# Kernel optimization log

Measured on AMD Instinct MI355X. Metric: run time of the kernel, lower is better.

## Reference

```python
import jax, jax.numpy as jnp
import numpy as np

EPS = 1e-5  # torch BatchNorm2d default eps


def _conv(x, w, b, pad):
    y = jax.lax.conv_general_dilated(
        x, w, window_strides=(1, 1), padding=[(pad, pad), (pad, pad)],
        dimension_numbers=('NCHW', 'OIHW', 'NCHW'))
    return y + b[None, :, None, None]


def _bn_train(x, gamma, beta):
    # training-mode BatchNorm2d: biased batch statistics over (N,H,W)
    m = jnp.mean(x, axis=(0, 2, 3), keepdims=True)
    v = jnp.var(x, axis=(0, 2, 3), keepdims=True)
    xn = (x - m) * jax.lax.rsqrt(v + EPS)
    return xn * gamma[None, :, None, None] + beta[None, :, None, None]


def _ncc(s, t):
    # Vectorized equivalent of the per-pixel double loop.
    # ncc[b,0,i,j] = mean(tt * ss / (tt_std * ss_std)) over (C,th,tw)
    #             = sum(tt * s_sub) / (N * tt_std * ss_std)   (since sum(tt)=0)
    b, c, sh, sw = s.shape
    th, tw = t.shape[2], t.shape[3]
    N = c * th * tw
    tt = t - jnp.mean(t, axis=(1, 2, 3), keepdims=True)
    # torch.std is unbiased (divides by N-1)
    tt_std = jnp.sqrt(jnp.sum(tt * tt, axis=(1, 2, 3), keepdims=True) / (N - 1))

    # cross[b] = valid correlation of s[b] with its own template tt[b]
    def per_sample(si, ti):
        return jax.lax.conv_general_dilated(
            si[None], ti[None], (1, 1), 'VALID',
            dimension_numbers=('NCHW', 'OIHW', 'NCHW'))[0]  # (1,h,w)

    cross = jax.vmap(per_sample)(s, tt)  # (b,1,h,w)

    # per-window mean/std of s via box-filter conv over all C channels jointly
    box = jnp.ones((1, c, th, tw), dtype=s.dtype)
    win_sum = jax.lax.conv_general_dilated(
        s, box, (1, 1), 'VALID', dimension_numbers=('NCHW', 'OIHW', 'NCHW'))
    win_sqsum = jax.lax.conv_general_dilated(
        s * s, box, (1, 1), 'VALID', dimension_numbers=('NCHW', 'OIHW', 'NCHW'))
    win_mean = win_sum / N
    ss_var = jnp.maximum(win_sqsum - N * win_mean * win_mean, 0.0) / (N - 1)
    ss_std = jnp.sqrt(ss_var)

    return cross / (N * tt_std * ss_std)  # (b,1,h,w)


def reference(s, t, w1, b1, g1, be1, w2, b2, g2, be2,
              w3, b3, g3, be3, w4, b4):
    s = _bn_train(_conv(s, w1, b1, pad=1), g1, be1)
    t = _bn_train(_conv(t, w2, b2, pad=1), g2, be2)
    ncc = _ncc(s, t)
    x = _bn_train(_conv(ncc, w3, b3, pad=0), g3, be3)
    x = jax.nn.relu(x)
    return _conv(x, w4, b4, pad=0)  # (b,2,h,w)


def setup_inputs() -> dict:
    key = jax.random.key(0)
    ks = jax.random.split(key, 12)
    C = 256
    inp = {
        's': jax.random.normal(ks[0], (16, C, 64, 64), jnp.float32),
        't': jax.random.normal(ks[1], (16, C, 16, 16), jnp.float32),
        'w1': jax.random.normal(ks[2], (C, C, 3, 3), jnp.float32) * 0.02,
        'b1': jax.random.normal(ks[3], (C,), jnp.float32) * 0.02,
        'g1': jnp.ones((C,), jnp.float32),
        'be1': jnp.zeros((C,), jnp.float32),
        'w2': jax.random.normal(ks[4], (C, C, 3, 3), jnp.float32) * 0.02,
        'b2': jax.random.normal(ks[5], (C,), jnp.float32) * 0.02,
        'g2': jnp.ones((C,), jnp.float32),
        'be2': jnp.zeros((C,), jnp.float32),
        'w3': jax.random.normal(ks[6], (1, 1, 1, 1), jnp.float32),
        'b3': jax.random.normal(ks[7], (1,), jnp.float32) * 0.02,
        'g3': jnp.ones((1,), jnp.float32),
        'be3': jnp.zeros((1,), jnp.float32),
        'w4': jax.random.normal(ks[8], (2, 1, 1, 1), jnp.float32),
        'b4': jax.random.normal(ks[9], (2,), jnp.float32) * 0.02,
    }
    return inp
```

## Files before the change

### kernel.cpp

```cpp
#include <hip/hip_runtime.h>
#include <hip/hip_bf16.h>

#define EPSV 1e-5f

constexpr int B_ = 16, C_ = 256;
constexpr int OHW_ = 49 * 49;
constexpr int NTOT = 256 * 16 * 16;
constexpr int GROUPS = 32, CPERG = 8;

typedef short bf16x8 __attribute__((ext_vector_type(8)));
typedef float f32x4 __attribute__((ext_vector_type(4)));

constexpr size_t OFF_S1 = 0;
constexpr size_t SZ_S1  = (size_t)16 * 256 * 4096;
constexpr size_t OFF_T2 = OFF_S1 + SZ_S1;
constexpr size_t SZ_T2  = (size_t)16 * 256 * 256;
constexpr size_t OFF_ST = OFF_T2 + SZ_T2;
constexpr size_t OFF_C  = OFF_ST + 2048;
constexpr size_t SPC_BYTES = (size_t)16 * 66 * 66 * 256 * 2;
constexpr size_t TPC_BYTES = (size_t)16 * 18 * 18 * 256 * 2;
constexpr size_t WR_BYTES  = (size_t)9 * 256 * 256 * 2;
constexpr size_t ZOFF  = 0;
constexpr size_t CPOFF = 131072;
constexpr size_t NCOFF = CPOFF + (size_t)GROUPS * 16 * OHW_;
constexpr size_t SATOFF = NCOFF + (size_t)16 * OHW_;

__device__ __forceinline__ void gload_lds16(const void* g, void* l) {
    __builtin_amdgcn_global_load_lds((const __attribute__((address_space(1))) unsigned int*)g,
                                     (__attribute__((address_space(3))) unsigned int*)l,
                                     16, 0, 0);
}

template<int W>
__global__ __launch_bounds__(256)
void pad_transpose(const float* __restrict__ in, __hip_bfloat16* __restrict__ outp)
{
    constexpr int PW = W + 2;
    __shared__ float tile[64][W + 1];
    int bid = blockIdx.x;
    int icg = bid & 3; bid >>= 2;
    int yp = bid % PW; bid /= PW;
    int b = bid;
    int ic0 = icg * 64;
    int tid = threadIdx.x;
    bool interior = (yp >= 1 && yp <= W);
    if (interior) {
        int y = yp - 1;
        for (int idx = tid; idx < 64 * W; idx += 256) {
            int i = idx / W, x = idx % W;
            tile[i][x] = in[(((size_t)(b * C_ + ic0 + i)) * W + y) * W + x];
        }
    }
    __syncthreads();
    for (int idx = tid; idx < PW * 16; idx += 256) {
        int xp = idx >> 4, i4 = idx & 15;
        ushort4 v = make_ushort4(0, 0, 0, 0);
        if (interior && xp >= 1 && xp <= W) {
            #pragma unroll
            for (int k = 0; k < 4; ++k) {
                __hip_bfloat16 h = __float2bfloat16(tile[i4 * 4 + k][xp - 1]);
                reinterpret_cast<unsigned short*>(&v)[k] = *reinterpret_cast<unsigned short*>(&h);
            }
        }
        *reinterpret_cast<ushort4*>(&outp[(((size_t)(b * PW) + yp) * PW + xp) * 256 + ic0 + i4 * 4]) = v;
    }
}

__global__ __launch_bounds__(256)
void weight_reorg(const float* __restrict__ w, __hip_bfloat16* __restrict__ wr)
{
    int idx = blockIdx.x * 256 + threadIdx.x;
    const float* src = w + (size_t)idx * 9;
    #pragma unroll
    for (int t = 0; t < 9; ++t)
        wr[(size_t)t * 65536 + idx] = __float2bfloat16(src[t]);
}

template<int W>
__global__ __launch_bounds__(256, 3)
void conv_mfma(const __hip_bfloat16* __restrict__ SPc, const __hip_bfloat16* __restrict__ Wr,
               const float* __restrict__ bias, float* __restrict__ out,
               float* __restrict__ csum, float* __restrict__ csq)
{
    constexpr int PW = W + 2;
    constexpr int NPIX = W * W;
    constexpr int NT = NPIX / 128;
    constexpr int NWG = 16 * 2 * NT;
    constexpr int CHUNK = NWG / 8;
    constexpr int NK = 72;
    __shared__ __hip_bfloat16 A_lds[3][128 * 32];
    __shared__ __hip_bfloat16 B_lds[3][128 * 32];

    int logical = (blockIdx.x & 7) * CHUNK + (blockIdx.x >> 3);
    int nt = logical % NT; logical /= NT;
    int mt = logical & 1;  logical >>= 1;
    int b  = logical;
    int tid = threadIdx.x;
    int lane = tid & 63;
    int wv = tid >> 6, wm = wv >> 1, wn = wv & 1;
    int oc0 = mt * 128, p0 = nt * 128;

    f32x4 acc[4][4];
    #pragma unroll
    for (int i = 0; i < 4; ++i)
        #pragma unroll
        for (int j = 0; j < 4; ++j)
            #pragma unroll
            for (int r = 0; r < 4; ++r) acc[i][j][r] = 0.f;

    int colb = lane >> 4;
    int rA = lane & 15;

    const __hip_bfloat16* baseA[2];
    const __hip_bfloat16* baseB[2];
    #pragma unroll
    for (int it = 0; it < 2; ++it) {
        int sIdx = tid + it * 256;
        int row = sIdx >> 2, seg = sIdx & 3;
        baseA[it] = Wr + ((size_t)(oc0 + row)) * 256 + seg * 8;
        int p = p0 + row;
        int y = p / W, x = p % W;
        baseB[it] = SPc + (((size_t)(b * PW + y)) * PW + x) * 256 + seg * 8;
    }

    auto STAGE = [&](int buf, int kc) {
        int tap = kc >> 3, icc = kc & 7;
        int offA = tap * 65536 + icc * 32;
        int offB = ((tap / 3) * PW + (tap % 3)) * 256 + icc * 32;
        #pragma unroll
        for (int it = 0; it < 2; ++it) {
            int sIdx = tid + it * 256;
            gload_lds16(baseA[it] + offA, &A_lds[buf][sIdx * 8]);
            gload_lds16(baseB[it] + offB, &B_lds[buf][sIdx * 8]);
        }
    };

    STAGE(0, 0);
    STAGE(1, 1);

    for (int k = 0; k < NK; ++k) {
        int cur = k % 3;
        if (k + 2 < NK) { asm volatile("s_waitcnt vmcnt(4)" ::: "memory"); }
        else            { asm volatile("s_waitcnt vmcnt(0)" ::: "memory"); }
        __builtin_amdgcn_s_barrier();
        asm volatile("" ::: "memory");

        const bf16x8* Af = reinterpret_cast<const bf16x8*>(&A_lds[cur][0]);
        const bf16x8* Bf = reinterpret_cast<const bf16x8*>(&B_lds[cur][0]);
        bf16x8 a[4], bb[4];
        #pragma unroll
        for (int mi = 0; mi < 4; ++mi)
            a[mi] = Af[(wm * 64 + mi * 16 + rA) * 4 + colb];
        #pragma unroll
        for (int ni = 0; ni < 4; ++ni)
            bb[ni] = Bf[(wn * 64 + ni * 16 + rA) * 4 + colb];
        #pragma unroll
        for (int mi = 0; mi < 4; ++mi)
            #pragma unroll
            for (int ni = 0; ni < 4; ++ni)
                acc[mi][ni] = __builtin_amdgcn_mfma_f32_16x16x32_bf16(
                    a[mi], bb[ni], acc[mi][ni], 0, 0, 0);

        if (k + 2 < NK) STAGE((k + 2) % 3, k + 2);
    }

    #pragma unroll
    for (int mi = 0; mi < 4; ++mi) {
        int ocb = oc0 + wm * 64 + mi * 16 + (lane >> 4) * 4;
        #pragma unroll
        for (int r = 0; r < 4; ++r) {
            int oc = ocb + r;
            float bv = bias[oc];
            float* orow = out + ((size_t)(b * C_ + oc)) * NPIX;
            float s_oc = 0.f, q_oc = 0.f;
            #pragma unroll
            for (int ni = 0; ni < 4; ++ni) {
                int px = p0 + wn * 64 + ni * 16 + (lane & 15);
                float v = acc[mi][ni][r] + bv;
                orow[px] = v;
                s_oc += v; q_oc += v * v;
            }
            #pragma unroll
            for (int m_ = 1; m_ < 16; m_ <<= 1) {
                s_oc += __shfl_xor(s_oc, m_);
                q_oc += __shfl_xor(q_oc, m_);
            }
            if ((lane & 15) == 0) {
                atomicAdd(&csum[oc], s_oc);
                atomicAdd(&csq[oc], q_oc);
            }
        }
    }
}

__device__ inline void blk_reduce2(float& a, float& q, int tid) {
    #pragma unroll
    for (int off = 32; off > 0; off >>= 1) {
        a += __shfl_down(a, off);
        q += __shfl_down(q, off);
    }
    __shared__ float ra[4], rq[4];
    if ((tid & 63) == 0) { ra[tid >> 6] = a; rq[tid >> 6] = q; }
    __syncthreads();
    if (tid == 0) { a = ra[0] + ra[1] + ra[2] + ra[3]; q = rq[0] + rq[1] + rq[2] + rq[3]; }
}

__global__ __launch_bounds__(256)
void bn_norm(float* __restrict__ x, const float* __restrict__ csum,
             const float* __restrict__ csq, const float* __restrict__ g,
             const float* __restrict__ be, int HW, int total4, float inv_cnt)
{
    int i = blockIdx.x * 256 + threadIdx.x;
    if (i >= total4) return;
    int c = ((i * 4) / HW) % C_;
    float m = csum[c] * inv_cnt;
    float v = csq[c] * inv_cnt - m * m;
    float sc = rsqrtf(v + EPSV) * g[c];
    float sh = be[c] - m * sc;
    float4 val = reinterpret_cast<float4*>(x)[i];
    val.x = val.x * sc + sh;
    val.y = val.y * sc + sh;
    val.z = val.z * sc + sh;
    val.w = val.w * sc + sh;
    reinterpret_cast<float4*>(x)[i] = val;
}

__global__ __launch_bounds__(256)
void zplane_kernel(const float* __restrict__ s1, const float* __restrict__ csum,
                   const float* __restrict__ csq, const float* __restrict__ g1,
                   const float* __restrict__ be1, float* __restrict__ z)
{
    __shared__ float SC[256], SH[256];
    int tid = threadIdx.x;
    {
        float m = csum[tid] * (1.f / 65536.f);
        float v = csq[tid] * (1.f / 65536.f) - m * m;
        float sc = rsqrtf(v + EPSV) * g1[tid];
        SC[tid] = sc; SH[tid] = be1[tid] - m * sc;
    }
    __syncthreads();
    int i4 = blockIdx.x * 256 + tid;
    int b = i4 >> 10, p4 = i4 & 1023;
    const float4* base = reinterpret_cast<const float4*>(s1 + (size_t)b * (C_ * 4096)) + p4;
    float4 s = make_float4(0.f, 0.f, 0.f, 0.f);
    float4 q = make_float4(0.f, 0.f, 0.f, 0.f);
    for (int c = 0; c < C_; ++c) {
        float4 v = base[(size_t)c * 1024];
        float sc = SC[c], sh = SH[c];
        float vx = v.x * sc + sh, vy = v.y * sc + sh, vz = v.z * sc + sh, vw = v.w * sc + sh;
        s.x += vx; s.y += vy; s.z += vz; s.w += vw;
        q.x += vx * vx; q.y += vy * vy; q.z += vz * vz; q.w += vw * vw;
    }
    reinterpret_cast<float4*>(z)[i4] = s;
    reinterpret_cast<float4*>(z + 65536)[i4] = q;
}

__global__ __launch_bounds__(256)
void sat_kernel(const float* __restrict__ zin, float* __restrict__ sat)
{
    __shared__ float t[65][66];
    int pl = blockIdx.x;
    int tid = threadIdx.x;
    const float* src = zin + (size_t)pl * 4096;
    for (int idx = tid; idx < 4096; idx += 256) {
        int y = idx >> 6, x = idx & 63;
        t[y + 1][x + 1] = src[idx];
    }
    for (int idx = tid; idx < 65; idx += 256) { t[0][idx] = 0.f; t[idx][0] = 0.f; }
    __syncthreads();
    if (tid < 64) {
        float run = 0.f;
        for (int x = 1; x <= 64; ++x) { run += t[tid + 1][x]; t[tid + 1][x] = run; }
    }
    __syncthreads();
    if (tid < 64) {
        float run = 0.f;
        for (int y = 1; y <= 64; ++y) { run += t[y][tid + 1]; t[y][tid + 1] = run; }
    }
    __syncthreads();
    float* dst = sat + (size_t)pl * 4225;
    for (int idx = tid; idx < 4225; idx += 256) {
        int r = idx / 65, c = idx % 65;
        dst[idx] = t[r][c];
    }
}

__global__ __launch_bounds__(256)
void tstat_kernel(const float* __restrict__ t2, float* __restrict__ tmean, float* __restrict__ ttstd)
{
    int b = blockIdx.x, tid = threadIdx.x;
    const float* p = t2 + (size_t)b * NTOT;
    float s = 0.f, q = 0.f;
    for (int i = tid; i < NTOT; i += 256) { float v = p[i]; s += v; q += v * v; }
    blk_reduce2(s, q, tid);
    if (tid == 0) {
        float m = s / (float)NTOT;
        tmean[b] = m;
        ttstd[b] = sqrtf(fmaxf(q - (float)NTOT * m * m, 0.f) / (float)(NTOT - 1));
    }
}

__global__ __launch_bounds__(256, 2)
void cross_v3(const float* __restrict__ s1, const float* __restrict__ t2,
              const float* __restrict__ csum, const float* __restrict__ csq,
              const float* __restrict__ g1, const float* __restrict__ be1,
              float* __restrict__ cpart)
{
    __shared__ float4 spl4[1024];
    __shared__ float tpl[256];
    __shared__ float red[4][64][49];

    int g = blockIdx.x & (GROUPS - 1);
    int b = blockIdx.x / GROUPS;
    int tid = threadIdx.x;
    int phase = tid >> 6;
    int lane = tid & 63;
    int i = lane;
    int i_ld = i < 49 ? i : 48;

    float acc[49];
    #pragma unroll
    for (int j = 0; j < 49; ++j) acc[j] = 0.f;

    #pragma unroll 1
    for (int cc = 0; cc < CPERG; ++cc) {
        int c = g * CPERG + cc;
        float m = csum[c] * (1.f / 65536.f);
        float v = csq[c] * (1.f / 65536.f) - m * m;
        float sc = rsqrtf(v + EPSV) * g1[c];
        float sh = be1[c] - m * sc;
        __syncthreads();
        const float4* sp4 = reinterpret_cast<const float4*>(s1 + ((size_t)(b * C_ + c)) * 4096);
        #pragma unroll
        for (int k = 0; k < 4; ++k) {
            int gidx = tid + k * 256;
            float4 val = sp4[gidx];
            val.x = val.x * sc + sh; val.y = val.y * sc + sh;
            val.z = val.z * sc + sh; val.w = val.w * sc + sh;
            int row = gidx >> 4, jg = gidx & 15;
            spl4[row * 16 + (jg ^ (row & 7))] = val;
        }
        tpl[tid] = t2[((size_t)(b * C_ + c)) * 256 + tid];
        __syncthreads();
        #pragma unroll 1
        for (int tyl = 0; tyl < 4; ++tyl) {
            int ty = phase * 4 + tyl;
            int row = i_ld + ty;
            float r_[64];
            #pragma unroll
            for (int jg = 0; jg < 16; ++jg) {
                float4 v4 = spl4[row * 16 + (jg ^ (row & 7))];
                r_[jg * 4 + 0] = v4.x; r_[jg * 4 + 1] = v4.y;
                r_[jg * 4 + 2] = v4.z; r_[jg * 4 + 3] = v4.w;
            }
            float tt[16];
            const float4* tp4 = reinterpret_cast<const float4*>(&tpl[ty * 16]);
            #pragma unroll
            for (int k = 0; k < 4; ++k) {
                float4 tv = tp4[k];
                tt[k * 4 + 0] = tv.x; tt[k * 4 + 1] = tv.y;
                tt[k * 4 + 2] = tv.z; tt[k * 4 + 3] = tv.w;
            }
            #pragma unroll
            for (int tx = 0; tx < 16; ++tx)
                #pragma unroll
                for (int j = 0; j < 49; ++j)
                    acc[j] += tt[tx] * r_[j + tx];
        }
    }
    __syncthreads();
    if (i < 49) {
        #pragma unroll
        for (int j = 0; j < 49; ++j) red[phase][i][j] = acc[j];
    }
    __syncthreads();
    float* dst = cpart + ((size_t)(g * B_ + b)) * OHW_;
    for (int e = tid; e < OHW_; e += 256) {
        int ii = e / 49, jj = e - ii * 49;
        dst[e] = red[0][ii][jj] + red[1][ii][jj] + red[2][ii][jj] + red[3][ii][jj];
    }
}

__global__ __launch_bounds__(256)
void ncc_kernel(const float* __restrict__ cpart, const float* __restrict__ sat,
                const float* __restrict__ tmean, const float* __restrict__ ttstd,
                float* __restrict__ ncc, float* __restrict__ s3)
{
    int idx = blockIdx.x * 256 + threadIdx.x;
    float val = 0.f;
    if (idx < B_ * OHW_) {
        int b = idx / OHW_, r = idx - b * OHW_;
        int i = r / 49, j = r - i * 49;
        float cr = 0.f;
        #pragma unroll 4
        for (int g = 0; g < GROUPS; ++g) cr += cpart[((size_t)(g * B_ + b)) * OHW_ + r];
        const float* sz = sat + (size_t)b * 4225;
        const float* sq = sat + (size_t)(16 + b) * 4225;
        int a00 = i * 65 + j, a01 = i * 65 + j + 16;
        int a10 = (i + 16) * 65 + j, a11 = (i + 16) * 65 + j + 16;
        float wsum = sz[a11] - sz[a01] - sz[a10] + sz[a00];
        float wq   = sq[a11] - sq[a01] - sq[a10] + sq[a00];
        float crosst = cr - tmean[b] * wsum;
        float ssvar = fmaxf(wq - wsum * wsum * (1.f / 65536.f), 0.f) * (1.f / 65535.f);
        float ssstd = sqrtf(ssvar);
        val = crosst / (65536.f * ttstd[b] * ssstd);
        ncc[idx] = val;
    }
    float s = val, q = val * val;
    blk_reduce2(s, q, threadIdx.x);
    if (threadIdx.x == 0) { atomicAdd(&s3[0], s); atomicAdd(&s3[1], q); }
}

__global__ __launch_bounds__(256)
void final_kernel(const float* __restrict__ ncc, const float* __restrict__ s3,
                  const float* __restrict__ w3, const float* __restrict__ b3,
                  const float* __restrict__ g3, const float* __restrict__ be3,
                  const float* __restrict__ w4, const float* __restrict__ b4,
                  float* __restrict__ out)
{
    int idx = blockIdx.x * 256 + threadIdx.x;
    if (idx >= B_ * OHW_) return;
    constexpr float M = (float)(B_ * OHW_);
    float mn = s3[0] / M;
    float vn = s3[1] / M - mn * mn;
    float W3 = w3[0], B3 = b3[0];
    float my = W3 * mn + B3;
    float vy = W3 * W3 * vn;
    float sc = rsqrtf(vy + EPSV) * g3[0];
    float y = (W3 * ncc[idx] + B3 - my) * sc + be3[0];
    float h = fmaxf(y, 0.f);
    int b = idx / OHW_, r = idx - b * OHW_;
    out[((size_t)(b * 2 + 0)) * OHW_ + r] = h * w4[0] + b4[0];
    out[((size_t)(b * 2 + 1)) * OHW_ + r] = h * w4[1] + b4[1];
}

extern "C" void kernel_launch(void* const* d_in, const int* in_sizes, int n_in,
                              void* d_out, int out_size, void* d_ws, size_t ws_size,
                              hipStream_t stream)
{
    const float* s   = (const float*)d_in[0];
    const float* t   = (const float*)d_in[1];
    const float* w1  = (const float*)d_in[2];
    const float* b1  = (const float*)d_in[3];
    const float* g1  = (const float*)d_in[4];
    const float* be1 = (const float*)d_in[5];
    const float* w2  = (const float*)d_in[6];
    const float* b2  = (const float*)d_in[7];
    const float* g2  = (const float*)d_in[8];
    const float* be2 = (const float*)d_in[9];
    const float* w3  = (const float*)d_in[10];
    const float* b3  = (const float*)d_in[11];
    const float* g3  = (const float*)d_in[12];
    const float* be3 = (const float*)d_in[13];
    const float* w4  = (const float*)d_in[14];
    const float* b4  = (const float*)d_in[15];

    float* ws = (float*)d_ws;
    float* S1 = ws + OFF_S1;
    float* T2 = ws + OFF_T2;
    float* ST = ws + OFF_ST;
    float* CHS1 = ST + 0;
    float* CHQ1 = ST + 256;
    float* CHS2 = ST + 512;
    float* CHQ2 = ST + 768;
    float* S3   = ST + 1024;
    float* TM   = ST + 1040;
    float* TSD  = ST + 1056;

    char* Cb = (char*)(ws + OFF_C);
    __hip_bfloat16* SPc = (__hip_bfloat16*)Cb;
    __hip_bfloat16* TPc = (__hip_bfloat16*)(Cb + SPC_BYTES);
    __hip_bfloat16* Wr1 = (__hip_bfloat16*)(Cb + SPC_BYTES + TPC_BYTES);
    __hip_bfloat16* Wr2 = (__hip_bfloat16*)(Cb + SPC_BYTES + TPC_BYTES + WR_BYTES);
    float* Cf = (float*)Cb;
    float* Z   = Cf + ZOFF;
    float* CP  = Cf + CPOFF;
    float* NC  = Cf + NCOFF;
    float* SAT = Cf + SATOFF;

    hipMemsetAsync(ST, 0, 1026 * sizeof(float), stream);

    pad_transpose<64><<<dim3(16 * 66 * 4), dim3(256), 0, stream>>>(s, SPc);
    pad_transpose<16><<<dim3(16 * 18 * 4), dim3(256), 0, stream>>>(t, TPc);
    weight_reorg<<<dim3(256), dim3(256), 0, stream>>>(w1, Wr1);
    weight_reorg<<<dim3(256), dim3(256), 0, stream>>>(w2, Wr2);

    conv_mfma<64><<<dim3(16 * 2 * 32), dim3(256), 0, stream>>>(SPc, Wr1, b1, S1, CHS1, CHQ1);
    conv_mfma<16><<<dim3(16 * 2 * 2),  dim3(256), 0, stream>>>(TPc, Wr2, b2, T2, CHS2, CHQ2);

    bn_norm<<<dim3(1024), dim3(256), 0, stream>>>(T2, CHS2, CHQ2, g2, be2, 256, 262144, 1.f / 4096.f);
    tstat_kernel<<<dim3(16), dim3(256), 0, stream>>>(T2, TM, TSD);

    zplane_kernel<<<dim3(64), dim3(256), 0, stream>>>(S1, CHS1, CHQ1, g1, be1, Z);
    sat_kernel<<<dim3(32), dim3(256), 0, stream>>>(Z, SAT);

    cross_v3<<<dim3(16 * GROUPS), dim3(256), 0, stream>>>(S1, T2, CHS1, CHQ1, g1, be1, CP);
    ncc_kernel<<<dim3(151), dim3(256), 0, stream>>>(CP, SAT, TM, TSD, NC, S3);
    final_kernel<<<dim3(151), dim3(256), 0, stream>>>(NC, S3, w3, b3, g3, be3, w4, b4, (float*)d_out);
}
```

Measured before the change: 513.3 us.

## Merge launches, fuse z-plane sums into cross kernel, double-buffer conv

After: 453.4 us. 11.7% less time.

```diff
diff --git a/kernel.cpp b/kernel.cpp
--- a/kernel.cpp
+++ b/kernel.cpp
@@ -16,12 +16,12 @@
 constexpr size_t OFF_T2 = OFF_S1 + SZ_S1;
 constexpr size_t SZ_T2  = (size_t)16 * 256 * 256;
 constexpr size_t OFF_ST = OFF_T2 + SZ_T2;
-constexpr size_t OFF_C  = OFF_ST + 2048;
+constexpr size_t OFF_Z  = OFF_ST + 2048;
+constexpr size_t OFF_C  = OFF_Z + 131072;
 constexpr size_t SPC_BYTES = (size_t)16 * 66 * 66 * 256 * 2;
 constexpr size_t TPC_BYTES = (size_t)16 * 18 * 18 * 256 * 2;
 constexpr size_t WR_BYTES  = (size_t)9 * 256 * 256 * 2;
-constexpr size_t ZOFF  = 0;
-constexpr size_t CPOFF = 131072;
+constexpr size_t CPOFF = 0;
 constexpr size_t NCOFF = CPOFF + (size_t)GROUPS * 16 * OHW_;
 constexpr size_t SATOFF = NCOFF + (size_t)16 * OHW_;
 
@@ -32,12 +32,10 @@
 }
 
 template<int W>
-__global__ __launch_bounds__(256)
-void pad_transpose(const float* __restrict__ in, __hip_bfloat16* __restrict__ outp)
+__device__ __forceinline__ void pad_body(int bid, const float* __restrict__ in,
+                                         __hip_bfloat16* __restrict__ outp, float* tile)
 {
     constexpr int PW = W + 2;
-    __shared__ float tile[64][W + 1];
-    int bid = blockIdx.x;
     int icg = bid & 3; bid >>= 2;
     int yp = bid % PW; bid /= PW;
     int b = bid;
@@ -48,7 +46,7 @@
         int y = yp - 1;
         for (int idx = tid; idx < 64 * W; idx += 256) {
             int i = idx / W, x = idx % W;
-            tile[i][x] = in[(((size_t)(b * C_ + ic0 + i)) * W + y) * W + x];
+            tile[i * (W + 1) + x] = in[(((size_t)(b * C_ + ic0 + i)) * W + y) * W + x];
         }
     }
     __syncthreads();
@@ -58,7 +56,7 @@
         if (interior && xp >= 1 && xp <= W) {
             #pragma unroll
             for (int k = 0; k < 4; ++k) {
-                __hip_bfloat16 h = __float2bfloat16(tile[i4 * 4 + k][xp - 1]);
+                __hip_bfloat16 h = __float2bfloat16(tile[(i4 * 4 + k) * (W + 1) + xp - 1]);
                 reinterpret_cast<unsigned short*>(&v)[k] = *reinterpret_cast<unsigned short*>(&h);
             }
         }
@@ -67,9 +65,22 @@
 }
 
 __global__ __launch_bounds__(256)
-void weight_reorg(const float* __restrict__ w, __hip_bfloat16* __restrict__ wr)
-{
-    int idx = blockIdx.x * 256 + threadIdx.x;
+void pad_all(const float* __restrict__ s, const float* __restrict__ t,
+             __hip_bfloat16* __restrict__ SPc, __hip_bfloat16* __restrict__ TPc)
+{
+    __shared__ float tile[64 * 65];
+    if (blockIdx.x < 16 * 66 * 4) pad_body<64>(blockIdx.x, s, SPc, tile);
+    else                          pad_body<16>(blockIdx.x - 16 * 66 * 4, t, TPc, tile);
+}
+
+__global__ __launch_bounds__(256)
+void weight_reorg_all(const float* __restrict__ w1, const float* __restrict__ w2,
+                      __hip_bfloat16* __restrict__ wr1, __hip_bfloat16* __restrict__ wr2)
+{
+    int bb = blockIdx.x;
+    const float* w = (bb < 256) ? w1 : w2;
+    __hip_bfloat16* wr = (bb < 256) ? wr1 : wr2;
+    int idx = (bb & 255) * 256 + threadIdx.x;
     const float* src = w + (size_t)idx * 9;
     #pragma unroll
     for (int t = 0; t < 9; ++t)
@@ -77,21 +88,16 @@
 }
 
 template<int W>
-__global__ __launch_bounds__(256, 3)
-void conv_mfma(const __hip_bfloat16* __restrict__ SPc, const __hip_bfloat16* __restrict__ Wr,
-               const float* __restrict__ bias, float* __restrict__ out,
-               float* __restrict__ csum, float* __restrict__ csq)
+__device__ __forceinline__ void conv_body(
+    int logical,
+    const __hip_bfloat16* __restrict__ SPc, const __hip_bfloat16* __restrict__ Wr,
+    const float* __restrict__ bias, float* __restrict__ out,
+    float* __restrict__ csum, float* __restrict__ csq,
+    __hip_bfloat16 (&A_lds)[2][4096], __hip_bfloat16 (&B_lds)[2][4096])
 {
     constexpr int PW = W + 2;
     constexpr int NPIX = W * W;
     constexpr int NT = NPIX / 128;
-    constexpr int NWG = 16 * 2 * NT;
-    constexpr int CHUNK = NWG / 8;
-    constexpr int NK = 72;
-    __shared__ __hip_bfloat16 A_lds[3][128 * 32];
-    __shared__ __hip_bfloat16 B_lds[3][128 * 32];
-
-    int logical = (blockIdx.x & 7) * CHUNK + (blockIdx.x >> 3);
     int nt = logical % NT; logical /= NT;
     int mt = logical & 1;  logical >>= 1;
     int b  = logical;
@@ -108,9 +114,7 @@
             #pragma unroll
             for (int r = 0; r < 4; ++r) acc[i][j][r] = 0.f;
 
-    int colb = lane >> 4;
-    int rA = lane & 15;
-
+    int colb = lane >> 4, rA = lane & 15;
     const __hip_bfloat16* baseA[2];
     const __hip_bfloat16* baseB[2];
     #pragma unroll
@@ -136,14 +140,12 @@
     };
 
     STAGE(0, 0);
-    STAGE(1, 1);
-
-    for (int k = 0; k < NK; ++k) {
-        int cur = k % 3;
-        if (k + 2 < NK) { asm volatile("s_waitcnt vmcnt(4)" ::: "memory"); }
-        else            { asm volatile("s_waitcnt vmcnt(0)" ::: "memory"); }
-        __builtin_amdgcn_s_barrier();
-        asm volatile("" ::: "memory");
+    asm volatile("s_waitcnt vmcnt(0)" ::: "memory");
+    __syncthreads();
+
+    for (int kc = 0; kc < 72; ++kc) {
+        int cur = kc & 1;
+        if (kc + 1 < 72) STAGE(cur ^ 1, kc + 1);
 
         const bf16x8* Af = reinterpret_cast<const bf16x8*>(&A_lds[cur][0]);
         const bf16x8* Bf = reinterpret_cast<const bf16x8*>(&B_lds[cur][0]);
@@ -161,12 +163,12 @@
                 acc[mi][ni] = __builtin_amdgcn_mfma_f32_16x16x32_bf16(
                     a[mi], bb[ni], acc[mi][ni], 0, 0, 0);
 
-        if (k + 2 < NK) STAGE((k + 2) % 3, k + 2);
+        __syncthreads();
     }
 
     #pragma unroll
     for (int mi = 0; mi < 4; ++mi) {
-        int ocb = oc0 + wm * 64 + mi * 16 + (lane >> 4) * 4;
+        int ocb = oc0 + wm * 64 + mi * 16 + colb * 4;
         #pragma unroll
         for (int r = 0; r < 4; ++r) {
             int oc = ocb + r;
@@ -175,7 +177,7 @@
             float s_oc = 0.f, q_oc = 0.f;
             #pragma unroll
             for (int ni = 0; ni < 4; ++ni) {
-                int px = p0 + wn * 64 + ni * 16 + (lane & 15);
+                int px = p0 + wn * 64 + ni * 16 + rA;
                 float v = acc[mi][ni][r] + bv;
                 orow[px] = v;
                 s_oc += v; q_oc += v * v;
@@ -185,7 +187,7 @@
                 s_oc += __shfl_xor(s_oc, m_);
                 q_oc += __shfl_xor(q_oc, m_);
             }
-            if ((lane & 15) == 0) {
+            if (rA == 0) {
                 atomicAdd(&csum[oc], s_oc);
                 atomicAdd(&csq[oc], q_oc);
             }
@@ -193,6 +195,26 @@
     }
 }
 
+__global__ __launch_bounds__(256, 4)
+void conv_all(const __hip_bfloat16* __restrict__ SPc, const __hip_bfloat16* __restrict__ Wr1,
+              const float* __restrict__ b1, float* __restrict__ S1,
+              float* __restrict__ CHS1, float* __restrict__ CHQ1,
+              const __hip_bfloat16* __restrict__ TPc, const __hip_bfloat16* __restrict__ Wr2,
+              const float* __restrict__ b2, float* __restrict__ T2,
+              float* __restrict__ CHS2, float* __restrict__ CHQ2)
+{
+    __shared__ __hip_bfloat16 A_lds[2][4096];
+    __shared__ __hip_bfloat16 B_lds[2][4096];
+    int bid = blockIdx.x;
+    if (bid < 64) {
+        conv_body<16>(bid, TPc, Wr2, b2, T2, CHS2, CHQ2, A_lds, B_lds);
+    } else {
+        int l = bid - 64;
+        int logical = (l & 7) * 128 + (l >> 3);
+        conv_body<64>(logical, SPc, Wr1, b1, S1, CHS1, CHQ1, A_lds, B_lds);
+    }
+}
+
 __device__ inline void blk_reduce2(float& a, float& q, int tid) {
     #pragma unroll
     for (int off = 32; off > 0; off >>= 1) {
@@ -206,92 +228,32 @@
 }
 
 __global__ __launch_bounds__(256)
-void bn_norm(float* __restrict__ x, const float* __restrict__ csum,
-             const float* __restrict__ csq, const float* __restrict__ g,
-             const float* __restrict__ be, int HW, int total4, float inv_cnt)
-{
-    int i = blockIdx.x * 256 + threadIdx.x;
-    if (i >= total4) return;
-    int c = ((i * 4) / HW) % C_;
-    float m = csum[c] * inv_cnt;
-    float v = csq[c] * inv_cnt - m * m;
-    float sc = rsqrtf(v + EPSV) * g[c];
-    float sh = be[c] - m * sc;
-    float4 val = reinterpret_cast<float4*>(x)[i];
-    val.x = val.x * sc + sh;
-    val.y = val.y * sc + sh;
-    val.z = val.z * sc + sh;
-    val.w = val.w * sc + sh;
-    reinterpret_cast<float4*>(x)[i] = val;
-}
-
-__global__ __launch_bounds__(256)
-void zplane_kernel(const float* __restrict__ s1, const float* __restrict__ csum,
-                   const float* __restrict__ csq, const float* __restrict__ g1,
-                   const float* __restrict__ be1, float* __restrict__ z)
+void bn_t2_stats(float* __restrict__ T2, const float* __restrict__ csum,
+                 const float* __restrict__ csq, const float* __restrict__ g2,
+                 const float* __restrict__ be2, float* __restrict__ tmean,
+                 float* __restrict__ ttstd)
 {
     __shared__ float SC[256], SH[256];
-    int tid = threadIdx.x;
+    int b = blockIdx.x, tid = threadIdx.x;
     {
-        float m = csum[tid] * (1.f / 65536.f);
-        float v = csq[tid] * (1.f / 65536.f) - m * m;
-        float sc = rsqrtf(v + EPSV) * g1[tid];
-        SC[tid] = sc; SH[tid] = be1[tid] - m * sc;
-    }
-    __syncthreads();
-    int i4 = blockIdx.x * 256 + tid;
-    int b = i4 >> 10, p4 = i4 & 1023;
-    const float4* base = reinterpret_cast<const float4*>(s1 + (size_t)b * (C_ * 4096)) + p4;
-    float4 s = make_float4(0.f, 0.f, 0.f, 0.f);
-    float4 q = make_float4(0.f, 0.f, 0.f, 0.f);
-    for (int c = 0; c < C_; ++c) {
-        float4 v = base[(size_t)c * 1024];
+        float m = csum[tid] * (1.f / 4096.f);
+        float v = csq[tid] * (1.f / 4096.f) - m * m;
+        float sc = rsqrtf(v + EPSV) * g2[tid];
+        SC[tid] = sc; SH[tid] = be2[tid] - m * sc;
+    }
+    __syncthreads();
+    float4* p = reinterpret_cast<float4*>(T2 + (size_t)b * NTOT);
+    float s = 0.f, q = 0.f;
+    for (int i4 = tid; i4 < NTOT / 4; i4 += 256) {
+        int c = i4 >> 6;
         float sc = SC[c], sh = SH[c];
-        float vx = v.x * sc + sh, vy = v.y * sc + sh, vz = v.z * sc + sh, vw = v.w * sc + sh;
-        s.x += vx; s.y += vy; s.z += vz; s.w += vw;
-        q.x += vx * vx; q.y += vy * vy; q.z += vz * vz; q.w += vw * vw;
-    }
-    reinterpret_cast<float4*>(z)[i4] = s;
-    reinterpret_cast<float4*>(z + 65536)[i4] = q;
-}
-
-__global__ __launch_bounds__(256)
-void sat_kernel(const float* __restrict__ zin, float* __restrict__ sat)
-{
-    __shared__ float t[65][66];
-    int pl = blockIdx.x;
-    int tid = threadIdx.x;
-    const float* src = zin + (size_t)pl * 4096;
-    for (int idx = tid; idx < 4096; idx += 256) {
-        int y = idx >> 6, x = idx & 63;
-        t[y + 1][x + 1] = src[idx];
-    }
-    for (int idx = tid; idx < 65; idx += 256) { t[0][idx] = 0.f; t[idx][0] = 0.f; }
-    __syncthreads();
-    if (tid < 64) {
-        float run = 0.f;
-        for (int x = 1; x <= 64; ++x) { run += t[tid + 1][x]; t[tid + 1][x] = run; }
-    }
-    __syncthreads();
-    if (tid < 64) {
-        float run = 0.f;
-        for (int y = 1; y <= 64; ++y) { run += t[y][tid + 1]; t[y][tid + 1] = run; }
-    }
-    __syncthreads();
-    float* dst = sat + (size_t)pl * 4225;
-    for (int idx = tid; idx < 4225; idx += 256) {
-        int r = idx / 65, c = idx % 65;
-        dst[idx] = t[r][c];
-    }
-}
-
-__global__ __launch_bounds__(256)
-void tstat_kernel(const float* __restrict__ t2, float* __restrict__ tmean, float* __restrict__ ttstd)
-{
-    int b = blockIdx.x, tid = threadIdx.x;
-    const float* p = t2 + (size_t)b * NTOT;
-    float s = 0.f, q = 0.f;
-    for (int i = tid; i < NTOT; i += 256) { float v = p[i]; s += v; q += v * v; }
+        float4 v = p[i4];
+        v.x = v.x * sc + sh; v.y = v.y * sc + sh;
+        v.z = v.z * sc + sh; v.w = v.w * sc + sh;
+        s += v.x + v.y + v.z + v.w;
+        q += v.x * v.x + v.y * v.y + v.z * v.z + v.w * v.w;
+        p[i4] = v;
+    }
     blk_reduce2(s, q, tid);
     if (tid == 0) {
         float m = s / (float)NTOT;
@@ -304,7 +266,7 @@
 void cross_v3(const float* __restrict__ s1, const float* __restrict__ t2,
               const float* __restrict__ csum, const float* __restrict__ csq,
               const float* __restrict__ g1, const float* __restrict__ be1,
-              float* __restrict__ cpart)
+              float* __restrict__ cpart, float* __restrict__ z)
 {
     __shared__ float4 spl4[1024];
     __shared__ float tpl[256];
@@ -321,6 +283,12 @@
     float acc[49];
     #pragma unroll
     for (int j = 0; j < 49; ++j) acc[j] = 0.f;
+    float4 zs[4], zq[4];
+    #pragma unroll
+    for (int k = 0; k < 4; ++k) {
+        zs[k] = make_float4(0.f, 0.f, 0.f, 0.f);
+        zq[k] = make_float4(0.f, 0.f, 0.f, 0.f);
+    }
 
     #pragma unroll 1
     for (int cc = 0; cc < CPERG; ++cc) {
@@ -337,6 +305,9 @@
             float4 val = sp4[gidx];
             val.x = val.x * sc + sh; val.y = val.y * sc + sh;
             val.z = val.z * sc + sh; val.w = val.w * sc + sh;
+            zs[k].x += val.x; zs[k].y += val.y; zs[k].z += val.z; zs[k].w += val.w;
+            zq[k].x += val.x * val.x; zq[k].y += val.y * val.y;
+            zq[k].z += val.z * val.z; zq[k].w += val.w * val.w;
             int row = gidx >> 4, jg = gidx & 15;
             spl4[row * 16 + (jg ^ (row & 7))] = val;
         }
@@ -368,6 +339,16 @@
                     acc[j] += tt[tx] * r_[j + tx];
         }
     }
+    #pragma unroll
+    for (int k = 0; k < 4; ++k) {
+        int pxb = (tid + k * 256) * 4;
+        float* zb  = z + (size_t)b * 4096 + pxb;
+        float* z2b = z + 65536 + (size_t)b * 4096 + pxb;
+        atomicAdd(&zb[0], zs[k].x);  atomicAdd(&zb[1], zs[k].y);
+        atomicAdd(&zb[2], zs[k].z);  atomicAdd(&zb[3], zs[k].w);
+        atomicAdd(&z2b[0], zq[k].x); atomicAdd(&z2b[1], zq[k].y);
+        atomicAdd(&z2b[2], zq[k].z); atomicAdd(&z2b[3], zq[k].w);
+    }
     __syncthreads();
     if (i < 49) {
         #pragma unroll
@@ -378,6 +359,36 @@
     for (int e = tid; e < OHW_; e += 256) {
         int ii = e / 49, jj = e - ii * 49;
         dst[e] = red[0][ii][jj] + red[1][ii][jj] + red[2][ii][jj] + red[3][ii][jj];
+    }
+}
+
+__global__ __launch_bounds__(256)
+void sat_kernel(const float* __restrict__ zin, float* __restrict__ sat)
+{
+    __shared__ float t[65][66];
+    int pl = blockIdx.x;
+    int tid = threadIdx.x;
+    const float* src = zin + (size_t)pl * 4096;
+    for (int idx = tid; idx < 4096; idx += 256) {
+        int y = idx >> 6, x = idx & 63;
+        t[y + 1][x + 1] = src[idx];
+    }
+    for (int idx = tid; idx < 65; idx += 256) { t[0][idx] = 0.f; t[idx][0] = 0.f; }
+    __syncthreads();
+    if (tid < 64) {
+        float run = 0.f;
+        for (int x = 1; x <= 64; ++x) { run += t[tid + 1][x]; t[tid + 1][x] = run; }
+    }
+    __syncthreads();
+    if (tid < 64) {
+        float run = 0.f;
+        for (int y = 1; y <= 64; ++y) { run += t[y][tid + 1]; t[y][tid + 1] = run; }
+    }
+    __syncthreads();
+    float* dst = sat + (size_t)pl * 4225;
+    for (int idx = tid; idx < 4225; idx += 256) {
+        int r = idx / 65, c = idx % 65;
+        dst[idx] = t[r][c];
     }
 }
 
@@ -466,6 +477,7 @@
     float* S3   = ST + 1024;
     float* TM   = ST + 1040;
     float* TSD  = ST + 1056;
+    float* Z    = ws + OFF_Z;
 
     char* Cb = (char*)(ws + OFF_C);
     __hip_bfloat16* SPc = (__hip_bfloat16*)Cb;
@@ -473,28 +485,22 @@
     __hip_bfloat16* Wr1 = (__hip_bfloat16*)(Cb + SPC_BYTES + TPC_BYTES);
     __hip_bfloat16* Wr2 = (__hip_bfloat16*)(Cb + SPC_BYTES + TPC_BYTES + WR_BYTES);
     float* Cf = (float*)Cb;
-    float* Z   = Cf + ZOFF;
     float* CP  = Cf + CPOFF;
     float* NC  = Cf + NCOFF;
     float* SAT = Cf + SATOFF;
 
-    hipMemsetAsync(ST, 0, 1026 * sizeof(float), stream);
-
-    pad_transpose<64><<<dim3(16 * 66 * 4), dim3(256), 0, stream>>>(s, SPc);
-    pad_transpose<16><<<dim3(16 * 18 * 4), dim3(256), 0, stream>>>(t, TPc);
-    weight_reorg<<<dim3(256), dim3(256), 0, stream>>>(w1, Wr1);
-    weight_reorg<<<dim3(256), dim3(256), 0, stream>>>(w2, Wr2);
-
-    conv_mfma<64><<<dim3(16 * 2 * 32), dim3(256), 0, stream>>>(SPc, Wr1, b1, S1, CHS1, CHQ1);
-    conv_mfma<16><<<dim3(16 * 2 * 2),  dim3(256), 0, stream>>>(TPc, Wr2, b2, T2, CHS2, CHQ2);
-
-    bn_norm<<<dim3(1024), dim3(256), 0, stream>>>(T2, CHS2, CHQ2, g2, be2, 256, 262144, 1.f / 4096.f);
-    tstat_kernel<<<dim3(16), dim3(256), 0, stream>>>(T2, TM, TSD);
-
-    zplane_kernel<<<dim3(64), dim3(256), 0, stream>>>(S1, CHS1, CHQ1, g1, be1, Z);
+    hipMemsetAsync(ST, 0, (2048 + 131072) * sizeof(float), stream);
+
+    pad_all<<<dim3(16 * 66 * 4 + 16 * 18 * 4), dim3(256), 0, stream>>>(s, t, SPc, TPc);
+    weight_reorg_all<<<dim3(512), dim3(256), 0, stream>>>(w1, w2, Wr1, Wr2);
+
+    conv_all<<<dim3(64 + 1024), dim3(256), 0, stream>>>(SPc, Wr1, b1, S1, CHS1, CHQ1,
+                                                        TPc, Wr2, b2, T2, CHS2, CHQ2);
+
+    bn_t2_stats<<<dim3(16), dim3(256), 0, stream>>>(T2, CHS2, CHQ2, g2, be2, TM, TSD);
+
+    cross_v3<<<dim3(16 * GROUPS), dim3(256), 0, stream>>>(S1, T2, CHS1, CHQ1, g1, be1, CP, Z);
     sat_kernel<<<dim3(32), dim3(256), 0, stream>>>(Z, SAT);
-
-    cross_v3<<<dim3(16 * GROUPS), dim3(256), 0, stream>>>(S1, T2, CHS1, CHQ1, g1, be1, CP);
     ncc_kernel<<<dim3(151), dim3(256), 0, stream>>>(CP, SAT, TM, TSD, NC, S3);
     final_kernel<<<dim3(151), dim3(256), 0, stream>>>(NC, S3, w3, b3, g3, be3, w4, b4, (float*)d_out);
 }
```
